# Kernel tuning notes

Hardware: AMD Instinct MI355X
Metric: run time of the kernel (lower is better)

## Reference

```python
import jax, jax.numpy as jnp
import numpy as np

N_NODES = 100000
PAIRNORM_EPS = 1e-5


def add_self_loops(edge_index, n):
    loops = jnp.arange(n, dtype=edge_index.dtype)
    src = jnp.concatenate([edge_index[0], loops])
    dst = jnp.concatenate([edge_index[1], loops])
    return src, dst


def gcn_norm(src, dst, n):
    # symmetric normalization D^-1/2 (A+I) D^-1/2, degree over targets (PyG flow source_to_target)
    deg = jax.ops.segment_sum(jnp.ones(dst.shape, jnp.float32), dst, num_segments=n)
    dinv = jnp.where(deg > 0, jax.lax.rsqrt(deg), 0.0)
    return dinv[src] * dinv[dst]  # [E]


def gcn_conv(x, src, dst, norm, W, b, n):
    h = x @ W                                   # [N, out]
    msg = h[src] * norm[:, None]                # gather + scale
    out = jax.ops.segment_sum(msg, dst, num_segments=n)  # scatter-add
    return out + b


def pairnorm(x):
    xc = x - jnp.mean(x, axis=0, keepdims=True)
    scale = jax.lax.rsqrt(PAIRNORM_EPS + jnp.mean(jnp.sum(xc * xc, axis=-1)))
    return xc * scale


def setup_inputs() -> dict:
    key = jax.random.key(0)
    ks = jax.random.split(key, 8)
    n, e, d_in, d_h, n_cls = N_NODES, 3200000, 512, 32, 40
    return {
        "x": jax.random.normal(ks[0], (n, d_in), jnp.float32),
        "edge_index": jax.random.randint(ks[1], (2, e), 0, n, jnp.int64),
        "W0": jax.random.normal(ks[2], (d_in, d_h), jnp.float32) * (1.0 / np.sqrt(d_in)),
        "b0": jnp.zeros((d_h,), jnp.float32),
        "W1": jax.random.normal(ks[3], (d_h, d_h), jnp.float32) * (1.0 / np.sqrt(d_h)),
        "b1": jnp.zeros((d_h,), jnp.float32),
        "Wf": jax.random.normal(ks[4], (d_h, n_cls), jnp.float32) * (1.0 / np.sqrt(d_h)),
        "bf": jnp.zeros((n_cls,), jnp.float32),
    }


def reference(x, edge_index, W0, b0, W1, b1, Wf, bf):
    n = x.shape[0]
    # drop_edge keep_ratio = 1.0 -> all edges kept each layer
    src, dst = add_self_loops(edge_index, n)
    norm = gcn_norm(src, dst, n)
    h = gcn_conv(x, src, dst, norm, W0, b0, n)
    h = jax.nn.relu(pairnorm(h))
    h = gcn_conv(h, src, dst, norm, W1, b1, n)
    h = jax.nn.relu(pairnorm(h))
    out = gcn_conv(h, src, dst, norm, Wf, bf, n)
    return out
```

## Files before the change

### kernel.cpp

```cpp
#include <hip/hip_runtime.h>
#include <hip/hip_bf16.h>

typedef __attribute__((ext_vector_type(8))) short bf16x8;
typedef __attribute__((ext_vector_type(4))) float f32x4;

#define NPB 512
#define EPB 8192

static __device__ __forceinline__ short f2bf(float v) {
  __hip_bfloat16 b = __float2bfloat16(v);
  return __builtin_bit_cast(short, b);
}
static __device__ __forceinline__ float bf2f(unsigned short u) {
  union { unsigned u; float f; } c; c.u = (unsigned)u << 16; return c.f;
}

__global__ void zero_int(int* p, int n) {
  int i = blockIdx.x * blockDim.x + threadIdx.x;
  if (i < n) p[i] = 0;
}
__global__ void make_dinv2(const int* __restrict__ cnt, float* __restrict__ dinv, int n) {
  int i = blockIdx.x * blockDim.x + threadIdx.x;
  if (i < n) dinv[i] = rsqrtf(1.0f + (float)cnt[i]);
}

__global__ __launch_bounds__(256) void bucket_hist(const int* __restrict__ dst,
                                                   int* __restrict__ bucket_cnt, int e, int nb) {
  __shared__ int lh[256];
  int t = threadIdx.x;
  lh[t] = 0;
  __syncthreads();
  int c0 = blockIdx.x * EPB, c1 = min(c0 + EPB, e);
  for (int i = c0 + t; i < c1; i += 256) atomicAdd(&lh[dst[i] >> 9], 1);
  __syncthreads();
  if (t < nb && lh[t] > 0) atomicAdd(&bucket_cnt[t], lh[t]);
}
__global__ void bucket_scan(const int* __restrict__ bucket_cnt, int* __restrict__ base,
                            int* __restrict__ gcursor, int nb, int e) {
  __shared__ int s[256];
  int t = threadIdx.x;
  int v = (t < nb) ? bucket_cnt[t] : 0;
  s[t] = v;
  __syncthreads();
  for (int off = 1; off < 256; off <<= 1) {
    int val = (t >= off) ? s[t - off] : 0;
    __syncthreads();
    s[t] += val;
    __syncthreads();
  }
  if (t < nb) { int b = s[t] - v; base[t] = b; gcursor[t] = b; }
  if (t == 0) base[nb] = e;
}
__global__ __launch_bounds__(256) void bucket_partition(const int* __restrict__ src,
    const int* __restrict__ dst, int* __restrict__ gcursor, int* __restrict__ ebuf,
    int e, int nb) {
  __shared__ int lh[256];
  __shared__ int lbase[256];
  int t = threadIdx.x;
  lh[t] = 0;
  __syncthreads();
  int c0 = blockIdx.x * EPB, c1 = min(c0 + EPB, e);
  for (int i = c0 + t; i < c1; i += 256) atomicAdd(&lh[dst[i] >> 9], 1);
  __syncthreads();
  if (t < nb && lh[t] > 0) lbase[t] = atomicAdd(&gcursor[t], lh[t]);
  lh[t] = 0;
  __syncthreads();
  for (int i = c0 + t; i < c1; i += 256) {
    int d = dst[i], b = d >> 9;
    int r = atomicAdd(&lh[b], 1);
    ebuf[lbase[b] + r] = ((d & (NPB - 1)) << 17) | src[i];
  }
}
__global__ __launch_bounds__(256) void node_count(const int* __restrict__ ebuf,
    const int* __restrict__ base, int* __restrict__ cnt, float* __restrict__ dinv, int n) {
  __shared__ int lc[NPB];
  int b = blockIdx.x;
  for (int i = threadIdx.x; i < NPB; i += 256) lc[i] = 0;
  __syncthreads();
  int b0 = base[b], b1 = base[b + 1];
  for (int i = b0 + threadIdx.x; i < b1; i += 256) atomicAdd(&lc[ebuf[i] >> 17], 1);
  __syncthreads();
  int g0 = b * NPB;
  for (int i = threadIdx.x; i < NPB; i += 256)
    if (g0 + i < n) {
      int c = lc[i];
      cnt[g0 + i] = c;
      dinv[g0 + i] = rsqrtf(1.0f + (float)c);
    }
}
__global__ __launch_bounds__(256) void scan1(const int* __restrict__ cnt, int* __restrict__ excl,
                                             int* __restrict__ blksum, int n) {
  __shared__ int tsum[256];
  int t = threadIdx.x;
  int idx = blockIdx.x * 1024 + t * 4;
  int4 v = {0, 0, 0, 0};
  if (idx + 3 < n) v = *(const int4*)(cnt + idx);
  else {
    if (idx < n) v.x = cnt[idx];
    if (idx + 1 < n) v.y = cnt[idx + 1];
    if (idx + 2 < n) v.z = cnt[idx + 2];
    if (idx + 3 < n) v.w = cnt[idx + 3];
  }
  int s = v.x + v.y + v.z + v.w;
  tsum[t] = s;
  __syncthreads();
  for (int off = 1; off < 256; off <<= 1) {
    int val = (t >= off) ? tsum[t - off] : 0;
    __syncthreads();
    tsum[t] += val;
    __syncthreads();
  }
  int e0 = tsum[t] - s;
  if (idx < n) excl[idx] = e0;
  if (idx + 1 < n) excl[idx + 1] = e0 + v.x;
  if (idx + 2 < n) excl[idx + 2] = e0 + v.x + v.y;
  if (idx + 3 < n) excl[idx + 3] = e0 + v.x + v.y + v.z;
  if (t == 255) blksum[blockIdx.x] = tsum[255];
}
__global__ void scan2(const int* __restrict__ blksum, int* __restrict__ blkoff, int nb) {
  __shared__ int s[256];
  int t = threadIdx.x;
  int v0 = (t < nb) ? blksum[t] : 0;
  s[t] = v0;
  __syncthreads();
  for (int off = 1; off < 256; off <<= 1) {
    int val = (t >= off) ? s[t - off] : 0;
    __syncthreads();
    s[t] += val;
    __syncthreads();
  }
  if (t < nb) blkoff[t] = s[t] - v0;
}
__global__ void scan3(int* __restrict__ rowptr, const int* __restrict__ blkoff, int n, int e) {
  int i = blockIdx.x * blockDim.x + threadIdx.x;
  if (i < n) rowptr[i] += blkoff[i >> 10];
  if (i == 0) rowptr[n] = e;
}
__global__ __launch_bounds__(256) void bucket_scatter(const int* __restrict__ ebuf,
    const int* __restrict__ base, const int* __restrict__ rowptr,
    int* __restrict__ ssrc, int n) {
  __shared__ int lcur[NPB];
  int b = blockIdx.x;
  int g0 = b * NPB;
  for (int i = threadIdx.x; i < NPB; i += 256)
    lcur[i] = (g0 + i < n) ? rowptr[g0 + i] : 0;
  __syncthreads();
  int b0 = base[b], b1 = base[b + 1];
  for (int i = b0 + threadIdx.x; i < b1; i += 256) {
    int p = ebuf[i];
    int pos = atomicAdd(&lcur[p >> 17], 1);
    ssrc[pos] = p & 0x1FFFF;
  }
}

__global__ __launch_bounds__(256) void gemm0_mfma(
    const float* __restrict__ x, const float* __restrict__ W,
    const float* __restrict__ dinv, unsigned short* __restrict__ hb, int n) {
  __shared__ bf16x8 wp[2048];
  int tid = threadIdx.x;
  for (int s = tid; s < 2048; s += 256) {
    int ct = s >> 10, rem = s & 1023, ks = rem >> 6, lane = rem & 63;
    int r = lane & 15, half = lane >> 4;
    int k0 = ks * 32 + half * 8;
    bf16x8 tmp;
#pragma unroll
    for (int j = 0; j < 8; ++j)
      tmp[j] = f2bf(W[(k0 + j) * 32 + ct * 16 + r]);
    wp[s] = tmp;
  }
  __syncthreads();
  int wave = tid >> 6, lane = tid & 63;
  int rowbase = blockIdx.x * 64 + wave * 16;
  int r = lane & 15, half = lane >> 4;
  int arow = rowbase + r; if (arow > n - 1) arow = n - 1;
  const float* xr = x + (size_t)arow * 512 + half * 8;
  f32x4 acc0 = {0.f, 0.f, 0.f, 0.f}, acc1 = {0.f, 0.f, 0.f, 0.f};
#pragma unroll
  for (int ks = 0; ks < 16; ++ks) {
    f32x4 a0 = *(const f32x4*)(xr + ks * 32);
    f32x4 a1 = *(const f32x4*)(xr + ks * 32 + 4);
    bf16x8 af;
    af[0] = f2bf(a0[0]); af[1] = f2bf(a0[1]); af[2] = f2bf(a0[2]); af[3] = f2bf(a0[3]);
    af[4] = f2bf(a1[0]); af[5] = f2bf(a1[1]); af[6] = f2bf(a1[2]); af[7] = f2bf(a1[3]);
    acc0 = __builtin_amdgcn_mfma_f32_16x16x32_bf16(af, wp[ks * 64 + lane], acc0, 0, 0, 0);
    acc1 = __builtin_amdgcn_mfma_f32_16x16x32_bf16(af, wp[1024 + ks * 64 + lane], acc1, 0, 0, 0);
  }
#pragma unroll
  for (int rg = 0; rg < 4; ++rg) {
    int row = rowbase + half * 4 + rg;
    if (row < n) {
      float dv = dinv[row];
      hb[(size_t)row * 32 + r]      = (unsigned short)f2bf(acc0[rg] * dv);
      hb[(size_t)row * 32 + 16 + r] = (unsigned short)f2bf(acc1[rg] * dv);
    }
  }
}

__global__ __launch_bounds__(256) void agg_gather32(
    const unsigned short* __restrict__ hb, const float* __restrict__ dinv,
    const float* __restrict__ bias, const int* __restrict__ rowptr,
    const int* __restrict__ ssrc, float* __restrict__ out, int n) {
  int wid = (int)((blockIdx.x * 256u + threadIdx.x) >> 6);
  int lane = threadIdx.x & 63;
  if (wid >= n) return;
  int f = lane & 31, half = lane >> 5;
  int r0 = rowptr[wid], r1 = rowptr[wid + 1];
  float acc = 0.f;
  for (int base = r0; base < r1; base += 64) {
    int cnt = min(64, r1 - base);
    int idx = ssrc[base + min(lane, cnt - 1)];
    for (int g = 0; g < cnt; g += 16) {
#pragma unroll
      for (int u = 0; u < 8; ++u) {
        int k = g + half + 2 * u;
        int kc = min(k, cnt - 1);
        int s = __shfl(idx, kc, 64);
        float v = bf2f(hb[(size_t)s * 32 + f]);
        acc += (k < cnt) ? v : 0.f;
      }
    }
  }
  acc += __shfl_down(acc, 32, 64);
  if (lane < 32) {
    float self = bf2f(hb[(size_t)wid * 32 + f]);
    out[(size_t)wid * 32 + f] = bias[f] + dinv[wid] * (self + acc);
  }
}
__global__ __launch_bounds__(256) void agg_gather40(
    const unsigned short* __restrict__ hb, const float* __restrict__ dinv,
    const float* __restrict__ bias, const int* __restrict__ rowptr,
    const int* __restrict__ ssrc, float* __restrict__ out, int n) {
  int wid = (int)((blockIdx.x * 256u + threadIdx.x) >> 6);
  int lane = threadIdx.x & 63;
  if (wid >= n) return;
  int r0 = rowptr[wid], r1 = rowptr[wid + 1];
  float acc = 0.f;
  for (int base = r0; base < r1; base += 64) {
    int cnt = min(64, r1 - base);
    int idx = ssrc[base + min(lane, cnt - 1)];
    for (int g = 0; g < cnt; g += 8) {
#pragma unroll
      for (int u = 0; u < 8; ++u) {
        int k = g + u;
        int kc = min(k, cnt - 1);
        int s = __shfl(idx, kc, 64);
        float v = (lane < 40) ? bf2f(hb[(size_t)s * 40 + lane]) : 0.f;
        acc += (k < cnt) ? v : 0.f;
      }
    }
  }
  if (lane < 40) {
    float self = bf2f(hb[(size_t)wid * 40 + lane]);
    out[(size_t)wid * 40 + lane] = bias[lane] + dinv[wid] * (self + acc);
  }
}

__global__ void count_dst(const int* __restrict__ dst, int* __restrict__ cnt, int e) {
  int i = blockIdx.x * blockDim.x + threadIdx.x;
  if (i < e) atomicAdd(&cnt[dst[i]], 1);
}
template <int F>
__global__ void agg_init(const unsigned short* __restrict__ hb, const float* __restrict__ dinv,
                         const float* __restrict__ bias, float* __restrict__ out, int n) {
  int idx = blockIdx.x * blockDim.x + threadIdx.x;
  if (idx >= n * F) return;
  int i = idx / F, f = idx - i * F;
  out[idx] = bias[f] + bf2f(hb[idx]) * dinv[i];
}
template <int F>
__global__ void agg_edges(const unsigned short* __restrict__ hb, const float* __restrict__ dinv,
                          const int* __restrict__ src, const int* __restrict__ dst,
                          float* __restrict__ out, int e) {
  int t = blockIdx.x * blockDim.x + threadIdx.x;
  int edge = t / F, f = t - edge * F;
  if (edge >= e) return;
  int s = src[edge], d = dst[edge];
  atomicAdd(&out[d * F + f], bf2f(hb[s * F + f]) * dinv[d]);
}

__global__ void zero_stats(float* stats) {
  if (threadIdx.x < 128) stats[threadIdx.x] = 0.f;
}
__global__ void pn_stats(const float* __restrict__ x, float* __restrict__ stats, int n) {
  int tid = threadIdx.x;
  int gsize = gridDim.x * blockDim.x;
  float csum = 0.f, ssq = 0.f;
  for (int idx = blockIdx.x * blockDim.x + tid; idx < n * 32; idx += gsize) {
    float v = x[idx];
    csum += v; ssq += v * v;
  }
#pragma unroll
  for (int off = 32; off >= 1; off >>= 1) ssq += __shfl_down(ssq, off, 64);
  csum += __shfl_down(csum, 32, 64);
  __shared__ float scs[4 * 32];
  __shared__ float sss[4];
  int w = tid >> 6, lane = tid & 63;
  if (lane < 32) scs[w * 32 + lane] = csum;
  if (lane == 0) sss[w] = ssq;
  __syncthreads();
  if (tid < 32) atomicAdd(&stats[tid], scs[tid] + scs[32 + tid] + scs[64 + tid] + scs[96 + tid]);
  if (tid == 0) atomicAdd(&stats[32], sss[0] + sss[1] + sss[2] + sss[3]);
}
__global__ void pn_finalize(float* stats, float inv_n) {
  int f = threadIdx.x;
  float ssq = stats[32];
  float mu = (f < 32) ? stats[f] * inv_n : 0.f;
  float m2 = mu * mu;
#pragma unroll
  for (int off = 32; off >= 1; off >>= 1) m2 += __shfl_down(m2, off, 64);
  if (f < 32) stats[f] = mu;
  if (f == 0) stats[32] = rsqrtf(1e-5f + ssq * inv_n - m2);
}

template <int FOUT>
__global__ void gemm_small_pn(const float* __restrict__ x, const float* __restrict__ W,
                              const float* __restrict__ stats, const float* __restrict__ dinv,
                              unsigned short* __restrict__ outb, int n) {
  __shared__ float Ws[32 * FOUT];
  __shared__ float mu[32];
  __shared__ float ssc[1];
  int t = threadIdx.x;
  for (int i = t; i < 32 * FOUT; i += blockDim.x) Ws[i] = W[i];
  if (t < 32) mu[t] = stats[t];
  if (t == 32) ssc[0] = stats[32];
  __syncthreads();
  float s = ssc[0];
  int idx = blockIdx.x * blockDim.x + t;
  int i = idx / FOUT, c = idx - i * FOUT;
  if (i >= n) return;
  const float* xr = x + (size_t)i * 32;
  float acc = 0.f;
#pragma unroll
  for (int k = 0; k < 32; ++k) {
    float v = (xr[k] - mu[k]) * s;
    v = v > 0.f ? v : 0.f;
    acc += v * Ws[k * FOUT + c];
  }
  outb[(size_t)i * FOUT + c] = (unsigned short)f2bf(acc * dinv[i]);
}

static inline int cdiv(long long a, long long b) { return (int)((a + b - 1) / b); }

extern "C" void kernel_launch(void* const* d_in, const int* in_sizes, int n_in,
                              void* d_out, int out_size, void* d_ws, size_t ws_size,
                              hipStream_t stream) {
  const float* x   = (const float*)d_in[0];
  const int*   ei  = (const int*)d_in[1];
  const float* W0  = (const float*)d_in[2];
  const float* b0  = (const float*)d_in[3];
  const float* W1  = (const float*)d_in[4];
  const float* b1  = (const float*)d_in[5];
  const float* Wf  = (const float*)d_in[6];
  const float* bfi = (const float*)d_in[7];
  float* out = (float*)d_out;

  int n = in_sizes[0] / 512;
  int e = in_sizes[1] / 2;
  const int* src = ei;
  const int* dst = ei + e;

  char* ws = (char*)d_ws;
  size_t o = 0;
  auto alloc = [&](size_t bytes) { char* p = ws + o; o = (o + bytes + 255) & ~(size_t)255; return p; };
  int*   cnt   = (int*)alloc((size_t)n * 4);
  float* dinv  = (float*)alloc((size_t)n * 4);
  float* stats = (float*)alloc(512);
  char*  hbuf  = alloc((size_t)n * 40 * 4);
  size_t fallback_need = o;
  int*   rowptr = (int*)alloc((size_t)(n + 1) * 4);
  int*   blksum = (int*)alloc(1024);
  int*   blkoff = (int*)alloc(1024);
  int*   bucket_cnt  = (int*)alloc(256 * 4);
  int*   bucket_base = (int*)alloc(257 * 4);
  int*   gcursor     = (int*)alloc(256 * 4);
  int*   ssrc   = (int*)alloc((size_t)e * 4);
  size_t csr_need = o;

  int* ebuf = (int*)hbuf;
  unsigned short* hb   = (unsigned short*)hbuf;
  unsigned short* hb40 = (unsigned short*)hbuf;
  float* bufB = out;
  float* stats0 = stats;
  float* stats1 = stats + 64;

  int NBk = cdiv(n, NPB);
  int nb2 = cdiv(n, 1024);
  bool use_csr = (ws_size >= csr_need) && (n <= 131072) && (NBk <= 256) && (nb2 <= 256) &&
                 ((size_t)n * 40 * 4 >= (size_t)e * 4);

  if (use_csr) {
    zero_int<<<1, 256, 0, stream>>>(bucket_cnt, NBk);
    bucket_hist<<<cdiv(e, EPB), 256, 0, stream>>>(dst, bucket_cnt, e, NBk);
    bucket_scan<<<1, 256, 0, stream>>>(bucket_cnt, bucket_base, gcursor, NBk, e);
    bucket_partition<<<cdiv(e, EPB), 256, 0, stream>>>(src, dst, gcursor, ebuf, e, NBk);
    node_count<<<NBk, 256, 0, stream>>>(ebuf, bucket_base, cnt, dinv, n);
    scan1<<<nb2, 256, 0, stream>>>(cnt, rowptr, blksum, n);
    scan2<<<1, 256, 0, stream>>>(blksum, blkoff, nb2);
    scan3<<<cdiv(n, 256), 256, 0, stream>>>(rowptr, blkoff, n, e);
    bucket_scatter<<<NBk, 256, 0, stream>>>(ebuf, bucket_base, rowptr, ssrc, n);
  } else {
    zero_int<<<cdiv(n, 256), 256, 0, stream>>>(cnt, n);
    count_dst<<<cdiv(e, 256), 256, 0, stream>>>(dst, cnt, e);
    make_dinv2<<<cdiv(n, 256), 256, 0, stream>>>(cnt, dinv, n);
  }
  zero_stats<<<1, 128, 0, stream>>>(stats);

  gemm0_mfma<<<cdiv(n, 64), 256, 0, stream>>>(x, W0, dinv, hb, n);
  if (use_csr) {
    agg_gather32<<<cdiv(n, 4), 256, 0, stream>>>(hb, dinv, b0, rowptr, ssrc, bufB, n);
  } else {
    agg_init<32><<<cdiv((long long)n * 32, 256), 256, 0, stream>>>(hb, dinv, b0, bufB, n);
    agg_edges<32><<<cdiv((long long)e * 32, 256), 256, 0, stream>>>(hb, dinv, src, dst, bufB, e);
  }
  pn_stats<<<400, 256, 0, stream>>>(bufB, stats0, n);
  pn_finalize<<<1, 64, 0, stream>>>(stats0, 1.0f / n);

  gemm_small_pn<32><<<cdiv((long long)n * 32, 256), 256, 0, stream>>>(bufB, W1, stats0, dinv, hb, n);
  if (use_csr) {
    agg_gather32<<<cdiv(n, 4), 256, 0, stream>>>(hb, dinv, b1, rowptr, ssrc, bufB, n);
  } else {
    agg_init<32><<<cdiv((long long)n * 32, 256), 256, 0, stream>>>(hb, dinv, b1, bufB, n);
    agg_edges<32><<<cdiv((long long)e * 32, 256), 256, 0, stream>>>(hb, dinv, src, dst, bufB, e);
  }
  pn_stats<<<400, 256, 0, stream>>>(bufB, stats1, n);
  pn_finalize<<<1, 64, 0, stream>>>(stats1, 1.0f / n);

  gemm_small_pn<40><<<cdiv((long long)n * 40, 320), 320, 0, stream>>>(bufB, Wf, stats1, dinv, hb40, n);
  if (use_csr) {
    agg_gather40<<<cdiv(n, 4), 256, 0, stream>>>(hb40, dinv, bfi, rowptr, ssrc, out, n);
  } else {
    agg_init<40><<<cdiv((long long)n * 40, 256), 256, 0, stream>>>(hb40, dinv, bfi, out, n);
    agg_edges<40><<<cdiv((long long)e * 40, 256), 256, 0, stream>>>(hb40, dinv, src, dst, out, e);
  }
}
```

Baseline: 815.7 us.

## Aggregate before final projection and vectorize gather with 8-byte loads

The last layer now aggregates the 32-wide normalized features first and applies the 32x40 projection afterwards (A(XW) = (AX)W), so the final gather moves 32 bf16 features per edge instead of 40. The gather kernel is rewritten so each lane loads 4 bf16 values at once via uint2 and 8 edges are processed per wave step, followed by a cross-lane reduction. The cost is an extra fp32 buffer, an extra pass for pn_relu and a separate small GEMM after aggregation. The sum order also changes, which affects rounding.

```diff
diff --git a/kernel.cpp b/kernel.cpp
--- a/kernel.cpp
+++ b/kernel.cpp
@@ -196,62 +196,52 @@
   }
 }
 
-__global__ __launch_bounds__(256) void agg_gather32(
+__global__ __launch_bounds__(256) void agg_gather32v(
     const unsigned short* __restrict__ hb, const float* __restrict__ dinv,
     const float* __restrict__ bias, const int* __restrict__ rowptr,
     const int* __restrict__ ssrc, float* __restrict__ out, int n) {
+  const uint2* hbu2 = (const uint2*)hb;
   int wid = (int)((blockIdx.x * 256u + threadIdx.x) >> 6);
   int lane = threadIdx.x & 63;
   if (wid >= n) return;
-  int f = lane & 31, half = lane >> 5;
+  int p = lane & 7, q = lane >> 3;
   int r0 = rowptr[wid], r1 = rowptr[wid + 1];
-  float acc = 0.f;
+  f32x4 acc = {0.f, 0.f, 0.f, 0.f};
   for (int base = r0; base < r1; base += 64) {
     int cnt = min(64, r1 - base);
     int idx = ssrc[base + min(lane, cnt - 1)];
+#pragma unroll 1
     for (int g = 0; g < cnt; g += 16) {
 #pragma unroll
-      for (int u = 0; u < 8; ++u) {
-        int k = g + half + 2 * u;
-        int kc = min(k, cnt - 1);
-        int s = __shfl(idx, kc, 64);
-        float v = bf2f(hb[(size_t)s * 32 + f]);
-        acc += (k < cnt) ? v : 0.f;
+      for (int u = 0; u < 2; ++u) {
+        int k = g + q + 8 * u;
+        int s = __shfl(idx, min(k, cnt - 1), 64);
+        uint2 v = hbu2[(size_t)s * 8 + p];
+        float w = (k < cnt) ? 1.f : 0.f;
+        acc[0] += w * bf2f((unsigned short)(v.x & 0xffff));
+        acc[1] += w * bf2f((unsigned short)(v.x >> 16));
+        acc[2] += w * bf2f((unsigned short)(v.y & 0xffff));
+        acc[3] += w * bf2f((unsigned short)(v.y >> 16));
       }
     }
   }
-  acc += __shfl_down(acc, 32, 64);
-  if (lane < 32) {
-    float self = bf2f(hb[(size_t)wid * 32 + f]);
-    out[(size_t)wid * 32 + f] = bias[f] + dinv[wid] * (self + acc);
-  }
-}
-__global__ __launch_bounds__(256) void agg_gather40(
-    const unsigned short* __restrict__ hb, const float* __restrict__ dinv,
-    const float* __restrict__ bias, const int* __restrict__ rowptr,
-    const int* __restrict__ ssrc, float* __restrict__ out, int n) {
-  int wid = (int)((blockIdx.x * 256u + threadIdx.x) >> 6);
-  int lane = threadIdx.x & 63;
-  if (wid >= n) return;
-  int r0 = rowptr[wid], r1 = rowptr[wid + 1];
-  float acc = 0.f;
-  for (int base = r0; base < r1; base += 64) {
-    int cnt = min(64, r1 - base);
-    int idx = ssrc[base + min(lane, cnt - 1)];
-    for (int g = 0; g < cnt; g += 8) {
-#pragma unroll
-      for (int u = 0; u < 8; ++u) {
-        int k = g + u;
-        int kc = min(k, cnt - 1);
-        int s = __shfl(idx, kc, 64);
-        float v = (lane < 40) ? bf2f(hb[(size_t)s * 40 + lane]) : 0.f;
-        acc += (k < cnt) ? v : 0.f;
-      }
-    }
-  }
-  if (lane < 40) {
-    float self = bf2f(hb[(size_t)wid * 40 + lane]);
-    out[(size_t)wid * 40 + lane] = bias[lane] + dinv[wid] * (self + acc);
+#pragma unroll
+  for (int off = 8; off <= 32; off <<= 1) {
+    acc[0] += __shfl_down(acc[0], off, 64);
+    acc[1] += __shfl_down(acc[1], off, 64);
+    acc[2] += __shfl_down(acc[2], off, 64);
+    acc[3] += __shfl_down(acc[3], off, 64);
+  }
+  if (lane < 8) {
+    uint2 sv = hbu2[(size_t)wid * 8 + p];
+    f32x4 b4 = *(const f32x4*)(bias + 4 * p);
+    float di = dinv[wid];
+    f32x4 res;
+    res[0] = b4[0] + di * (bf2f((unsigned short)(sv.x & 0xffff)) + acc[0]);
+    res[1] = b4[1] + di * (bf2f((unsigned short)(sv.x >> 16))    + acc[1]);
+    res[2] = b4[2] + di * (bf2f((unsigned short)(sv.y & 0xffff)) + acc[2]);
+    res[3] = b4[3] + di * (bf2f((unsigned short)(sv.y >> 16))    + acc[3]);
+    *(f32x4*)(out + (size_t)wid * 32 + 4 * p) = res;
   }
 }
 
@@ -259,27 +249,25 @@
   int i = blockIdx.x * blockDim.x + threadIdx.x;
   if (i < e) atomicAdd(&cnt[dst[i]], 1);
 }
-template <int F>
-__global__ void agg_init(const unsigned short* __restrict__ hb, const float* __restrict__ dinv,
-                         const float* __restrict__ bias, float* __restrict__ out, int n) {
+__global__ void agg_init32(const unsigned short* __restrict__ hb, const float* __restrict__ dinv,
+                           const float* __restrict__ bias, float* __restrict__ out, int n) {
   int idx = blockIdx.x * blockDim.x + threadIdx.x;
-  if (idx >= n * F) return;
-  int i = idx / F, f = idx - i * F;
+  if (idx >= n * 32) return;
+  int i = idx >> 5, f = idx & 31;
   out[idx] = bias[f] + bf2f(hb[idx]) * dinv[i];
 }
-template <int F>
-__global__ void agg_edges(const unsigned short* __restrict__ hb, const float* __restrict__ dinv,
-                          const int* __restrict__ src, const int* __restrict__ dst,
-                          float* __restrict__ out, int e) {
+__global__ void agg_edges32(const unsigned short* __restrict__ hb, const float* __restrict__ dinv,
+                            const int* __restrict__ src, const int* __restrict__ dst,
+                            float* __restrict__ out, int e) {
   int t = blockIdx.x * blockDim.x + threadIdx.x;
-  int edge = t / F, f = t - edge * F;
+  int edge = t >> 5, f = t & 31;
   if (edge >= e) return;
   int s = src[edge], d = dst[edge];
-  atomicAdd(&out[d * F + f], bf2f(hb[s * F + f]) * dinv[d]);
+  atomicAdd(&out[d * 32 + f], bf2f(hb[s * 32 + f]) * dinv[d]);
 }
 
 __global__ void zero_stats(float* stats) {
-  if (threadIdx.x < 128) stats[threadIdx.x] = 0.f;
+  if (threadIdx.x < 192) stats[threadIdx.x] = 0.f;
 }
 __global__ void pn_stats(const float* __restrict__ x, float* __restrict__ stats, int n) {
   int tid = threadIdx.x;
@@ -312,21 +300,20 @@
   if (f == 0) stats[32] = rsqrtf(1e-5f + ssq * inv_n - m2);
 }
 
-template <int FOUT>
-__global__ void gemm_small_pn(const float* __restrict__ x, const float* __restrict__ W,
-                              const float* __restrict__ stats, const float* __restrict__ dinv,
-                              unsigned short* __restrict__ outb, int n) {
-  __shared__ float Ws[32 * FOUT];
+__global__ void gemm_small_pn32(const float* __restrict__ x, const float* __restrict__ W,
+                                const float* __restrict__ stats, const float* __restrict__ dinv,
+                                unsigned short* __restrict__ outb, int n) {
+  __shared__ float Ws[32 * 32];
   __shared__ float mu[32];
   __shared__ float ssc[1];
   int t = threadIdx.x;
-  for (int i = t; i < 32 * FOUT; i += blockDim.x) Ws[i] = W[i];
+  for (int i = t; i < 32 * 32; i += blockDim.x) Ws[i] = W[i];
   if (t < 32) mu[t] = stats[t];
   if (t == 32) ssc[0] = stats[32];
   __syncthreads();
   float s = ssc[0];
   int idx = blockIdx.x * blockDim.x + t;
-  int i = idx / FOUT, c = idx - i * FOUT;
+  int i = idx >> 5, c = idx & 31;
   if (i >= n) return;
   const float* xr = x + (size_t)i * 32;
   float acc = 0.f;
@@ -334,9 +321,42 @@
   for (int k = 0; k < 32; ++k) {
     float v = (xr[k] - mu[k]) * s;
     v = v > 0.f ? v : 0.f;
-    acc += v * Ws[k * FOUT + c];
-  }
-  outb[(size_t)i * FOUT + c] = (unsigned short)f2bf(acc * dinv[i]);
+    acc += v * Ws[k * 32 + c];
+  }
+  outb[(size_t)i * 32 + c] = (unsigned short)f2bf(acc * dinv[i]);
+}
+
+__global__ void pn_relu_bf16(const float* __restrict__ x, const float* __restrict__ stats,
+                             const float* __restrict__ dinv, unsigned short* __restrict__ outb, int n) {
+  __shared__ float mu[32];
+  __shared__ float ssc[1];
+  int t = threadIdx.x;
+  if (t < 32) mu[t] = stats[t];
+  if (t == 32) ssc[0] = stats[32];
+  __syncthreads();
+  float s = ssc[0];
+  int idx = blockIdx.x * blockDim.x + t;
+  if (idx >= n * 32) return;
+  int i = idx >> 5, f = idx & 31;
+  float v = (x[idx] - mu[f]) * s;
+  v = v > 0.f ? v : 0.f;
+  outb[idx] = (unsigned short)f2bf(v * dinv[i]);
+}
+
+__global__ void gemm_small40(const float* __restrict__ x, const float* __restrict__ W,
+                             const float* __restrict__ bias, float* __restrict__ out, int n) {
+  __shared__ float Ws[32 * 40];
+  int t = threadIdx.x;
+  for (int i = t; i < 32 * 40; i += blockDim.x) Ws[i] = W[i];
+  __syncthreads();
+  int idx = blockIdx.x * blockDim.x + t;
+  int i = idx / 40, c = idx - i * 40;
+  if (i >= n) return;
+  const float* xr = x + (size_t)i * 32;
+  float acc = 0.f;
+#pragma unroll
+  for (int k = 0; k < 32; ++k) acc += xr[k] * Ws[k * 40 + c];
+  out[(size_t)i * 40 + c] = acc + bias[c];
 }
 
 static inline int cdiv(long long a, long long b) { return (int)((a + b - 1) / b); }
@@ -364,8 +384,9 @@
   auto alloc = [&](size_t bytes) { char* p = ws + o; o = (o + bytes + 255) & ~(size_t)255; return p; };
   int*   cnt   = (int*)alloc((size_t)n * 4);
   float* dinv  = (float*)alloc((size_t)n * 4);
-  float* stats = (float*)alloc(512);
+  float* stats = (float*)alloc(1024);
   char*  hbuf  = alloc((size_t)n * 40 * 4);
+  float* bufC  = (float*)alloc((size_t)n * 32 * 4);
   size_t fallback_need = o;
   int*   rowptr = (int*)alloc((size_t)(n + 1) * 4);
   int*   blksum = (int*)alloc(1024);
@@ -377,11 +398,11 @@
   size_t csr_need = o;
 
   int* ebuf = (int*)hbuf;
-  unsigned short* hb   = (unsigned short*)hbuf;
-  unsigned short* hb40 = (unsigned short*)hbuf;
+  unsigned short* hb = (unsigned short*)hbuf;
   float* bufB = out;
   float* stats0 = stats;
   float* stats1 = stats + 64;
+  float* zbias  = stats + 128;
 
   int NBk = cdiv(n, NPB);
   int nb2 = cdiv(n, 1024);
@@ -403,33 +424,34 @@
     count_dst<<<cdiv(e, 256), 256, 0, stream>>>(dst, cnt, e);
     make_dinv2<<<cdiv(n, 256), 256, 0, stream>>>(cnt, dinv, n);
   }
-  zero_stats<<<1, 128, 0, stream>>>(stats);
+  zero_stats<<<1, 256, 0, stream>>>(stats);
 
   gemm0_mfma<<<cdiv(n, 64), 256, 0, stream>>>(x, W0, dinv, hb, n);
   if (use_csr) {
-    agg_gather32<<<cdiv(n, 4), 256, 0, stream>>>(hb, dinv, b0, rowptr, ssrc, bufB, n);
+    agg_gather32v<<<cdiv(n, 4), 256, 0, stream>>>(hb, dinv, b0, rowptr, ssrc, bufB, n);
   } else {
-    agg_init<32><<<cdiv((long long)n * 32, 256), 256, 0, stream>>>(hb, dinv, b0, bufB, n);
-    agg_edges<32><<<cdiv((long long)e * 32, 256), 256, 0, stream>>>(hb, dinv, src, dst, bufB, e);
+    agg_init32<<<cdiv((long long)n * 32, 256), 256, 0, stream>>>(hb, dinv, b0, bufB, n);
+    agg_edges32<<<cdiv((long long)e * 32, 256), 256, 0, stream>>>(hb, dinv, src, dst, bufB, e);
   }
   pn_stats<<<400, 256, 0, stream>>>(bufB, stats0, n);
   pn_finalize<<<1, 64, 0, stream>>>(stats0, 1.0f / n);
 
-  gemm_small_pn<32><<<cdiv((long long)n * 32, 256), 256, 0, stream>>>(bufB, W1, stats0, dinv, hb, n);
+  gemm_small_pn32<<<cdiv((long long)n * 32, 256), 256, 0, stream>>>(bufB, W1, stats0, dinv, hb, n);
   if (use_csr) {
-    agg_gather32<<<cdiv(n, 4), 256, 0, stream>>>(hb, dinv, b1, rowptr, ssrc, bufB, n);
+    agg_gather32v<<<cdiv(n, 4), 256, 0, stream>>>(hb, dinv, b1, rowptr, ssrc, bufB, n);
   } else {
-    agg_init<32><<<cdiv((long long)n * 32, 256), 256, 0, stream>>>(hb, dinv, b1, bufB, n);
-    agg_edges<32><<<cdiv((long long)e * 32, 256), 256, 0, stream>>>(hb, dinv, src, dst, bufB, e);
+    agg_init32<<<cdiv((long long)n * 32, 256), 256, 0, stream>>>(hb, dinv, b1, bufB, n);
+    agg_edges32<<<cdiv((long long)e * 32, 256), 256, 0, stream>>>(hb, dinv, src, dst, bufB, e);
   }
   pn_stats<<<400, 256, 0, stream>>>(bufB, stats1, n);
   pn_finalize<<<1, 64, 0, stream>>>(stats1, 1.0f / n);
 
-  gemm_small_pn<40><<<cdiv((long long)n * 40, 320), 320, 0, stream>>>(bufB, Wf, stats1, dinv, hb40, n);
+  pn_relu_bf16<<<cdiv((long long)n * 32, 256), 256, 0, stream>>>(bufB, stats1, dinv, hb, n);
   if (use_csr) {
-    agg_gather40<<<cdiv(n, 4), 256, 0, stream>>>(hb40, dinv, bfi, rowptr, ssrc, out, n);
+    agg_gather32v<<<cdiv(n, 4), 256, 0, stream>>>(hb, dinv, zbias, rowptr, ssrc, bufC, n);
   } else {
-    agg_init<40><<<cdiv((long long)n * 40, 256), 256, 0, stream>>>(hb40, dinv, bfi, out, n);
-    agg_edges<40><<<cdiv((long long)e * 40, 256), 256, 0, stream>>>(hb40, dinv, src, dst, out, e);
-  }
-}
+    agg_init32<<<cdiv((long long)n * 32, 256), 256, 0, stream>>>(hb, dinv, zbias, bufC, n);
+    agg_edges32<<<cdiv((long long)e * 32, 256), 256, 0, stream>>>(hb, dinv, src, dst, bufC, e);
+  }
+  gemm_small40<<<cdiv((long long)n * 40, 320), 320, 0, stream>>>(bufC, Wf, bfi, out, n);
+}
```

Result: faster. 669.8 us (-17.9%).
